# Kernel optimization log

Measured on AMD Instinct MI355X. Metric: run time of the kernel, lower is better.

Reference implementation:

```python
import jax, jax.numpy as jnp
import numpy as np
from jax import lax

DIM = 256
HEADS = 8


def dwconv3x3(x, w, b):
    # x: [B,C,H,W], w: [C,1,3,3] depthwise (groups=C), b: [C]
    y = lax.conv_general_dilated(
        x, w, window_strides=(1, 1), padding='SAME',
        dimension_numbers=('NCHW', 'OIHW', 'NCHW'),
        feature_group_count=x.shape[1])
    return y + b[None, :, None, None]


def conv1x1(x, w, b):
    # x: [B,Cin,H,W], w: [Cout,Cin], b: [Cout]
    return jnp.einsum('oc,bchw->bohw', w, x) + b[None, :, None, None]


def setup_inputs() -> dict:
    key = jax.random.key(0)
    ks = jax.random.split(key, 12)
    s = 0.05
    inp = {
        'x': jax.random.normal(ks[0], (4, DIM, 128, 128), dtype=jnp.float32),
        'q_w': jax.random.normal(ks[1], (DIM, 1, 3, 3), dtype=jnp.float32) * s,
        'q_b': jax.random.normal(ks[2], (DIM,), dtype=jnp.float32) * s,
        'k_w': jax.random.normal(ks[3], (DIM, 1, 3, 3), dtype=jnp.float32) * s,
        'k_b': jax.random.normal(ks[4], (DIM,), dtype=jnp.float32) * s,
        'v_w': jax.random.normal(ks[5], (DIM, 1, 3, 3), dtype=jnp.float32) * s,
        'v_b': jax.random.normal(ks[6], (DIM,), dtype=jnp.float32) * s,
        'out_w': jax.random.normal(ks[7], (DIM, DIM), dtype=jnp.float32) * s,
        'out_b': jax.random.normal(ks[8], (DIM,), dtype=jnp.float32) * s,
        'fusion_w': jax.random.normal(ks[9], (DIM, 2 * DIM), dtype=jnp.float32) * s,
        'fusion_b': jax.random.normal(ks[10], (DIM,), dtype=jnp.float32) * s,
        'temperature': jnp.ones((HEADS, 1, 1), dtype=jnp.float32),
        'gamma': jax.random.normal(ks[11], (1,), dtype=jnp.float32) * 0.1,
    }
    return inp


def reference(x, q_w, q_b, k_w, k_b, v_w, v_b, out_w, out_b,
              fusion_w, fusion_b, temperature, gamma):
    b, c, h, w = x.shape
    ch = c // HEADS  # channels per head (32)
    q = dwconv3x3(x, q_w, q_b).reshape(b, HEADS, ch, h * w)
    k = dwconv3x3(x, k_w, k_b).reshape(b, HEADS, ch, h * w)
    v = dwconv3x3(x, v_w, v_b).reshape(b, HEADS, ch, h * w)
    # channel-wise attention: [b, head, c, c]
    attn = jnp.einsum('bhcn,bhdn->bhcd', q, k) * temperature[None]
    attn = jax.nn.softmax(attn, axis=-1)
    out = jnp.einsum('bhcd,bhdn->bhcn', attn, v).reshape(b, c, h, w)
    out = conv1x1(out, out_w, out_b)
    fused = jnp.concatenate([out * gamma[0], x], axis=1)  # [b, 2c, h, w]
    return conv1x1(fused, fusion_w, fusion_b)
```

## Files before the change

### kernel.cpp

```cpp
#include <hip/hip_runtime.h>

typedef __attribute__((ext_vector_type(8))) short bf16x8;
typedef __attribute__((ext_vector_type(4))) float f32x4;

static __device__ __forceinline__ unsigned short f2bf(float f) {
  unsigned u = __builtin_bit_cast(unsigned, f);
  unsigned r = u + 0x7fffu + ((u >> 16) & 1u);
  return (unsigned short)(r >> 16);
}
static __device__ __forceinline__ unsigned pkbf(float a, float b) {
  return (unsigned)f2bf(a) | ((unsigned)f2bf(b) << 16);
}

__global__ __launch_bounds__(256) void kprep(
    const float* __restrict__ out_w, const float* __restrict__ out_b,
    const float* __restrict__ fusion_w, const float* __restrict__ fusion_b,
    const float* __restrict__ gamma,
    float* __restrict__ W1g, float* __restrict__ bias_tot,
    unsigned short* __restrict__ Wcat) {
  const int o = blockIdx.x;
  const int c = threadIdx.x;
  const float g = gamma[0];
  float acc = 0.f, bacc = 0.f;
  for (int t = 0; t < 256; ++t) {
    float fw = fusion_w[o*512 + t];
    acc  += fw * out_w[t*256 + c];
    bacc += fw * out_b[t];
  }
  W1g[o*256 + c] = g * acc;
  if (c == 0) bias_tot[o] = g * bacc + fusion_b[o];
  unsigned short w2b = f2bf(fusion_w[o*512 + 256 + c]);
  const int col = ((c >> 5) << 6) + 32 + (c & 31);
  for (int b = 0; b < 4; ++b)
    Wcat[((size_t)(b*256 + o))*512 + col] = w2b;
}

struct SmA { float xs[5184]; unsigned short qk[2][32][256]; };
union SmU { SmA a; unsigned short vx[256][72]; };

__global__ __launch_bounds__(256, 3) void k_qkv(
    const float* __restrict__ x,
    const float* __restrict__ q_w, const float* __restrict__ q_b,
    const float* __restrict__ k_w, const float* __restrict__ k_b,
    const float* __restrict__ v_w, const float* __restrict__ v_b,
    unsigned short* __restrict__ bx,
    float* __restrict__ gp)
{
  __shared__ SmU sm;
  const int t = blockIdx.x, h = blockIdx.y, b = blockIdx.z;
  const int tid = threadIdx.x;
  __builtin_assume(tid < 256);
  const int wv = tid >> 6, lane = tid & 63;
  const int w4 = __builtin_amdgcn_readfirstlane(wv);
  const int ty = t >> 3, tx = t & 7;
  const int y0 = ty * 16, x0 = tx * 16;
  const int py = lane >> 2, px0 = (lane & 3) * 4;

  float ra[21], rb[21];
  #pragma unroll
  for (int it = 0; it < 21; ++it) {
    int i = tid + it * 256;
    ra[it] = 0.f; rb[it] = 0.f;
    if (i < 5184) {
      int c = i / 324, r = i - c * 324;
      int yy = r / 18, xx = r - yy * 18;
      int gy = y0 + yy - 1, gx = x0 + xx - 1;
      if ((unsigned)gy < 128u && (unsigned)gx < 128u) {
        const float* p = x + (((size_t)(b * 256 + h * 32 + c)) * 128 + gy) * 128 + gx;
        ra[it] = p[0];
        rb[it] = p[16 * 16384];
      }
    }
  }

  uint2 vpack[2][4], xpack[2][4];
  #pragma unroll
  for (int pass = 0; pass < 2; ++pass) {
    #pragma unroll
    for (int it = 0; it < 21; ++it) {
      int i = tid + it * 256;
      if (i < 5184) sm.a.xs[i] = pass ? rb[it] : ra[it];
    }
    __syncthreads();

    const int cbase = h * 32 + pass * 16;
    float vvf[4][4], xxf[4][4];
    #pragma unroll
    for (int j = 0; j < 4; ++j) {
      const int cl = w4 * 4 + j;
      const int ch = cbase + cl;
      float wq[9], wk[9], wvv[9];
      #pragma unroll
      for (int i2 = 0; i2 < 9; ++i2) {
        wq[i2]  = q_w[ch * 9 + i2];
        wk[i2]  = k_w[ch * 9 + i2];
        wvv[i2] = v_w[ch * 9 + i2];
      }
      const float bq = q_b[ch], bk = k_b[ch], bv = v_b[ch];
      float win[3][6];
      #pragma unroll
      for (int r = 0; r < 3; ++r) {
        const float* xrow = &sm.a.xs[cl * 324 + (py + r) * 18 + px0];
        float2 a01 = *(const float2*)&xrow[0];
        float2 a23 = *(const float2*)&xrow[2];
        float2 a45 = *(const float2*)&xrow[4];
        win[r][0] = a01.x; win[r][1] = a01.y;
        win[r][2] = a23.x; win[r][3] = a23.y;
        win[r][4] = a45.x; win[r][5] = a45.y;
      }
      const int ah = pass * 16 + cl;
      float q4[4], k4[4];
      #pragma unroll
      for (int px = 0; px < 4; ++px) {
        float aq = bq, ak = bk, av = bv;
        #pragma unroll
        for (int r = 0; r < 3; ++r)
          #pragma unroll
          for (int cx = 0; cx < 3; ++cx) {
            float xv = win[r][px + cx];
            aq += wq[r * 3 + cx] * xv;
            ak += wk[r * 3 + cx] * xv;
            av += wvv[r * 3 + cx] * xv;
          }
        q4[px] = aq; k4[px] = ak;
        vvf[j][px] = av;
        xxf[j][px] = win[1][px + 1];
      }
      const int sw = (((lane >> 1) ^ (ah & 7)) << 3) + ((lane & 1) << 2);
      *(uint2*)&sm.a.qk[0][ah][sw] = make_uint2(pkbf(q4[0], q4[1]), pkbf(q4[2], q4[3]));
      *(uint2*)&sm.a.qk[1][ah][sw] = make_uint2(pkbf(k4[0], k4[1]), pkbf(k4[2], k4[3]));
    }
    #pragma unroll
    for (int px = 0; px < 4; ++px) {
      vpack[pass][px] = make_uint2(pkbf(vvf[0][px], vvf[1][px]), pkbf(vvf[2][px], vvf[3][px]));
      xpack[pass][px] = make_uint2(pkbf(xxf[0][px], xxf[1][px]), pkbf(xxf[2][px], xxf[3][px]));
    }
    __syncthreads();
  }

  const int qm = wv >> 1, qn = wv & 1;
  const int lrow = lane & 15, quad = lane >> 4;
  const int rowa = qm * 16 + lrow, rowb = qn * 16 + lrow;
  f32x4 acc = {0.f, 0.f, 0.f, 0.f};
  #pragma unroll
  for (int ks = 0; ks < 8; ++ks) {
    bf16x8 a  = *(const bf16x8*)&sm.a.qk[0][rowa][(((ks * 4 + quad) ^ (rowa & 7)) << 3)];
    bf16x8 bb = *(const bf16x8*)&sm.a.qk[1][rowb][(((ks * 4 + quad) ^ (rowb & 7)) << 3)];
    acc = __builtin_amdgcn_mfma_f32_16x16x32_bf16(a, bb, acc, 0, 0, 0);
  }
  float* gpb = gp + ((size_t)((b * 8 + h) * 64 + t)) * 1024;
  #pragma unroll
  for (int r = 0; r < 4; ++r)
    gpb[(qm * 16 + quad * 4 + r) * 32 + qn * 16 + lrow] = acc[r];

  __syncthreads();

  const int chi = wv >> 1, half = wv & 1;
  #pragma unroll
  for (int pass = 0; pass < 2; ++pass)
    #pragma unroll
    for (int px = 0; px < 4; ++px) {
      int n = py * 16 + px0 + px;
      int key = (n >> 3) & 7;
      int cv = pass * 2 + chi;
      int cx2 = 4 + pass * 2 + chi;
      *(uint2*)&sm.vx[n][((cv ^ key) << 3) + (half << 2)] = vpack[pass][px];
      *(uint2*)&sm.vx[n][((cx2 ^ key) << 3) + (half << 2)] = xpack[pass][px];
    }
  __syncthreads();

  #pragma unroll
  for (int it = 0; it < 8; ++it) {
    int n = it * 32 + (tid >> 3);
    int m = tid & 7;
    int key = (n >> 3) & 7;
    uint4 val = *(const uint4*)&sm.vx[n][((m ^ key) << 3)];
    int pyn = n >> 4, pxn = n & 15;
    int ng = (y0 + pyn) * 128 + x0 + pxn;
    *(uint4*)&bx[((size_t)b * 16384 + ng) * 512 + h * 64 + m * 8] = val;
  }
}

__global__ __launch_bounds__(1024) void k_red(
    const float* __restrict__ gp, float* __restrict__ gp2) {
  const int g = blockIdx.x, h = blockIdx.y, b = blockIdx.z;
  const int tid = threadIdx.x;
  const float* base = gp + ((size_t)((b * 8 + h) * 64 + g * 8)) * 1024;
  float s = 0.f;
  #pragma unroll
  for (int t = 0; t < 8; ++t) s += base[t * 1024 + tid];
  gp2[((size_t)((b * 8 + h) * 8 + g)) * 1024 + tid] = s;
}

__global__ __launch_bounds__(1024) void k_softmax(
    const float* __restrict__ gp2, const float* __restrict__ temp,
    float* __restrict__ attn) {
  const int h = blockIdx.x, b = blockIdx.y;
  const int tid = threadIdx.x;
  const int c = tid >> 5, d = tid & 31;
  const float* base = gp2 + ((size_t)((b*8 + h)*8))*1024;
  float s = 0.f;
  #pragma unroll
  for (int t = 0; t < 8; ++t) s += base[t*1024 + tid];
  s *= temp[h];
  __shared__ float ls[32][33];
  ls[c][d] = s;
  __syncthreads();
  float m = -1e30f;
  #pragma unroll
  for (int i = 0; i < 32; ++i) m = fmaxf(m, ls[c][i]);
  __syncthreads();
  float e = __expf(s - m);
  ls[c][d] = e;
  __syncthreads();
  float sum = 0.f;
  #pragma unroll
  for (int i = 0; i < 32; ++i) sum += ls[c][i];
  attn[((size_t)((b*8 + h)*32 + c))*32 + d] = e / sum;
}

__global__ __launch_bounds__(256) void k_compose(
    const float* __restrict__ W1g, const float* __restrict__ attn,
    unsigned short* __restrict__ Wcat) {
  const int o = blockIdx.x, b = blockIdx.y;
  const int e = threadIdx.x;
  const int h = e >> 5, d = e & 31;
  const float* ab = attn + ((size_t)((b*8 + h)*32))*32 + d;
  const float* wb = W1g + o*256 + h*32;
  float s = 0.f;
  #pragma unroll
  for (int c2 = 0; c2 < 32; ++c2) s += wb[c2] * ab[c2*32];
  Wcat[((size_t)(b*256 + o))*512 + ((e >> 5) << 6) + (e & 31)] = f2bf(s);
}

__global__ __launch_bounds__(256) void k_gemm(
    const unsigned short* __restrict__ Wcat,
    const unsigned short* __restrict__ bx,
    const float* __restrict__ bias_tot,
    float* __restrict__ out) {
  __shared__ unsigned short Al[256][40];
  __shared__ unsigned short Bl[64][40];
  const int nt = blockIdx.x, b = blockIdx.y;
  const int tid = threadIdx.x;
  const int wv = tid >> 6, lane = tid & 63;
  const int lrow = lane & 15, quad = lane >> 4;
  const int nbase = nt * 64;
  const unsigned short* Ab = Wcat + (size_t)b * 256 * 512;
  const unsigned short* Bb = bx + ((size_t)b * 16384 + nbase) * 512;
  f32x4 acc[4][4] = {};

  const int srow = tid >> 2;
  const int sq4 = tid & 3;
  for (int ks = 0; ks < 16; ++ks) {
    const int k0 = ks * 32;
    #pragma unroll
    for (int r = 0; r < 4; ++r) {
      int row = srow + r*64;
      uint4 v4 = *(const uint4*)(Ab + (size_t)row*512 + k0 + sq4*8);
      *(uint4*)&Al[row][sq4*8] = v4;
    }
    {
      uint4 v4 = *(const uint4*)(Bb + (size_t)srow*512 + k0 + sq4*8);
      *(uint4*)&Bl[srow][sq4*8] = v4;
    }
    __syncthreads();
    bf16x8 af[4], bfv[4];
    #pragma unroll
    for (int i = 0; i < 4; ++i)
      af[i] = *(const bf16x8*)&Al[wv*64 + i*16 + lrow][quad*8];
    #pragma unroll
    for (int j = 0; j < 4; ++j)
      bfv[j] = *(const bf16x8*)&Bl[j*16 + lrow][quad*8];
    #pragma unroll
    for (int i = 0; i < 4; ++i)
      #pragma unroll
      for (int j = 0; j < 4; ++j)
        acc[i][j] = __builtin_amdgcn_mfma_f32_16x16x32_bf16(af[i], bfv[j], acc[i][j], 0, 0, 0);
    __syncthreads();
  }
  #pragma unroll
  for (int i = 0; i < 4; ++i) {
    #pragma unroll
    for (int r = 0; r < 4; ++r) {
      const int o = wv*64 + i*16 + quad*4 + r;
      const float bias = bias_tot[o];
      #pragma unroll
      for (int j = 0; j < 4; ++j) {
        const int n = nbase + j*16 + lrow;
        out[((size_t)(b*256 + o))*16384 + n] = acc[i][j][r] + bias;
      }
    }
  }
}

extern "C" void kernel_launch(void* const* d_in, const int* in_sizes, int n_in,
                              void* d_out, int out_size, void* d_ws, size_t ws_size,
                              hipStream_t stream) {
  const float* x        = (const float*)d_in[0];
  const float* q_w      = (const float*)d_in[1];
  const float* q_b      = (const float*)d_in[2];
  const float* k_w      = (const float*)d_in[3];
  const float* k_b      = (const float*)d_in[4];
  const float* v_w      = (const float*)d_in[5];
  const float* v_b      = (const float*)d_in[6];
  const float* out_w    = (const float*)d_in[7];
  const float* out_b    = (const float*)d_in[8];
  const float* fusion_w = (const float*)d_in[9];
  const float* fusion_b = (const float*)d_in[10];
  const float* temp     = (const float*)d_in[11];
  const float* gamma    = (const float*)d_in[12];
  float* out = (float*)d_out;

  char* ws = (char*)d_ws;
  unsigned short* bx   = (unsigned short*)(ws);
  float* gp            = (float*)(ws + 67108864);
  float* attn          = (float*)(ws + 75497472);
  float* W1g           = (float*)(ws + 75628544);
  float* bias_tot      = (float*)(ws + 75890688);
  unsigned short* Wcat = (unsigned short*)(ws + 75891712);
  float* gp2           = (float*)(ws + 76940288);

  kprep<<<dim3(256), dim3(256), 0, stream>>>(out_w, out_b, fusion_w, fusion_b,
                                             gamma, W1g, bias_tot, Wcat);
  k_qkv<<<dim3(64, 8, 4), dim3(256), 0, stream>>>(x, q_w, q_b, k_w, k_b, v_w, v_b, bx, gp);
  k_red<<<dim3(8, 8, 4), dim3(1024), 0, stream>>>(gp, gp2);
  k_softmax<<<dim3(8, 4), dim3(1024), 0, stream>>>(gp2, temp, attn);
  k_compose<<<dim3(256, 4), dim3(256), 0, stream>>>(W1g, attn, Wcat);
  k_gemm<<<dim3(256, 4), dim3(256), 0, stream>>>(Wcat, bx, bias_tot, out);
}
```

Before: 228.5 us.

## Load conv windows directly from global memory and shrink LDS for higher occupancy

The depthwise QKV conv kernel no longer stages the haloed input tile in shared memory. Each thread reads its 3x6 window straight from global memory, with a templated interior/border split so interior tiles skip bounds checks. The V/X transpose buffer is halved and written out in two rounds, and launch bounds are raised to 4 blocks per CU. The intent is to cut LDS traffic, barriers and register pressure so more blocks fit per CU. In exchange it does redundant overlapping global loads that rely on the cache hierarchy, plus an extra pair of barriers in the store phase.

```diff
diff --git a/kernel.cpp b/kernel.cpp
--- a/kernel.cpp
+++ b/kernel.cpp
@@ -35,10 +35,100 @@
     Wcat[((size_t)(b*256 + o))*512 + col] = w2b;
 }
 
-struct SmA { float xs[5184]; unsigned short qk[2][32][256]; };
-union SmU { SmA a; unsigned short vx[256][72]; };
-
-__global__ __launch_bounds__(256, 3) void k_qkv(
+struct SmQK { unsigned short qk[2][32][256]; };
+union SmU { SmQK a; unsigned short vx[128][72]; };
+
+template<bool BORDER>
+static __device__ __forceinline__ void conv_passes(
+    const float* __restrict__ x,
+    const float* __restrict__ q_w, const float* __restrict__ q_b,
+    const float* __restrict__ k_w, const float* __restrict__ k_b,
+    const float* __restrict__ v_w, const float* __restrict__ v_b,
+    SmU& sm, int b, int h, int w4, int lane,
+    int y0, int x0, int py, int px0,
+    uint2 vpack[2][4], uint2 xpack[2][4]) {
+  const int gy_base = y0 + py - 1;
+  const int gxc = x0 + px0;
+  const bool vr0 = !BORDER || ((unsigned)gy_base < 128u);
+  const bool vr2 = !BORDER || ((unsigned)(gy_base + 2) < 128u);
+  const bool gl  = !BORDER || (gxc > 0);
+  const bool gr  = !BORDER || (gxc + 4 < 128);
+
+  #pragma unroll
+  for (int pass = 0; pass < 2; ++pass) {
+    const int cbase = h * 32 + pass * 16;
+    #pragma unroll
+    for (int j = 0; j < 4; ++j) {
+      const int cl = w4 * 4 + j;
+      const int ch = cbase + cl;
+      float wq[9], wk[9], wvv[9];
+      #pragma unroll
+      for (int i2 = 0; i2 < 9; ++i2) {
+        wq[i2]  = q_w[ch * 9 + i2];
+        wk[i2]  = k_w[ch * 9 + i2];
+        wvv[i2] = v_w[ch * 9 + i2];
+      }
+      const float bq = q_b[ch], bk = k_b[ch], bv = v_b[ch];
+      const float* p = x + (((size_t)(b * 256 + ch)) * 128 + gy_base) * 128 + gxc;
+      float win[3][6];
+      #pragma unroll
+      for (int r = 0; r < 3; ++r) {
+        const float* pr = p + r * 128;
+        const bool vr = (r == 0) ? vr0 : (r == 2 ? vr2 : true);
+        if (!BORDER) {
+          float4 m4 = *(const float4*)pr;
+          win[r][0] = pr[-1];
+          win[r][1] = m4.x; win[r][2] = m4.y; win[r][3] = m4.z; win[r][4] = m4.w;
+          win[r][5] = pr[4];
+        } else {
+          float4 m4 = vr ? *(const float4*)pr : make_float4(0.f, 0.f, 0.f, 0.f);
+          win[r][0] = (vr && gl) ? pr[-1] : 0.f;
+          win[r][1] = m4.x; win[r][2] = m4.y; win[r][3] = m4.z; win[r][4] = m4.w;
+          win[r][5] = (vr && gr) ? pr[4] : 0.f;
+        }
+      }
+      const int ah = pass * 16 + cl;
+      float q4[4], k4[4], v4[4];
+      #pragma unroll
+      for (int px = 0; px < 4; ++px) {
+        float aq = bq, ak = bk, av = bv;
+        #pragma unroll
+        for (int r = 0; r < 3; ++r)
+          #pragma unroll
+          for (int cx = 0; cx < 3; ++cx) {
+            float xv = win[r][px + cx];
+            aq += wq[r * 3 + cx] * xv;
+            ak += wk[r * 3 + cx] * xv;
+            av += wvv[r * 3 + cx] * xv;
+          }
+        q4[px] = aq; k4[px] = ak; v4[px] = av;
+      }
+      const int sw = (((lane >> 1) ^ (ah & 7)) << 3) + ((lane & 1) << 2);
+      *(uint2*)&sm.a.qk[0][ah][sw] = make_uint2(pkbf(q4[0], q4[1]), pkbf(q4[2], q4[3]));
+      *(uint2*)&sm.a.qk[1][ah][sw] = make_uint2(pkbf(k4[0], k4[1]), pkbf(k4[2], k4[3]));
+      if (j == 0 || j == 2) {
+        #pragma unroll
+        for (int px = 0; px < 4; ++px) {
+          if (j == 0) { vpack[pass][px].x = pkbf(v4[px], 0.f); xpack[pass][px].x = pkbf(win[1][px + 1], 0.f); }
+          else        { vpack[pass][px].y = pkbf(v4[px], 0.f); xpack[pass][px].y = pkbf(win[1][px + 1], 0.f); }
+        }
+      } else {
+        #pragma unroll
+        for (int px = 0; px < 4; ++px) {
+          if (j == 1) {
+            vpack[pass][px].x |= (unsigned)f2bf(v4[px]) << 16;
+            xpack[pass][px].x |= (unsigned)f2bf(win[1][px + 1]) << 16;
+          } else {
+            vpack[pass][px].y |= (unsigned)f2bf(v4[px]) << 16;
+            xpack[pass][px].y |= (unsigned)f2bf(win[1][px + 1]) << 16;
+          }
+        }
+      }
+    }
+  }
+}
+
+__global__ __launch_bounds__(256, 4) void k_qkv(
     const float* __restrict__ x,
     const float* __restrict__ q_w, const float* __restrict__ q_b,
     const float* __restrict__ k_w, const float* __restrict__ k_b,
@@ -55,88 +145,15 @@
   const int ty = t >> 3, tx = t & 7;
   const int y0 = ty * 16, x0 = tx * 16;
   const int py = lane >> 2, px0 = (lane & 3) * 4;
-
-  float ra[21], rb[21];
-  #pragma unroll
-  for (int it = 0; it < 21; ++it) {
-    int i = tid + it * 256;
-    ra[it] = 0.f; rb[it] = 0.f;
-    if (i < 5184) {
-      int c = i / 324, r = i - c * 324;
-      int yy = r / 18, xx = r - yy * 18;
-      int gy = y0 + yy - 1, gx = x0 + xx - 1;
-      if ((unsigned)gy < 128u && (unsigned)gx < 128u) {
-        const float* p = x + (((size_t)(b * 256 + h * 32 + c)) * 128 + gy) * 128 + gx;
-        ra[it] = p[0];
-        rb[it] = p[16 * 16384];
-      }
-    }
-  }
+  const bool border = (ty == 0) || (ty == 7) || (tx == 0) || (tx == 7);
 
   uint2 vpack[2][4], xpack[2][4];
-  #pragma unroll
-  for (int pass = 0; pass < 2; ++pass) {
-    #pragma unroll
-    for (int it = 0; it < 21; ++it) {
-      int i = tid + it * 256;
-      if (i < 5184) sm.a.xs[i] = pass ? rb[it] : ra[it];
-    }
-    __syncthreads();
-
-    const int cbase = h * 32 + pass * 16;
-    float vvf[4][4], xxf[4][4];
-    #pragma unroll
-    for (int j = 0; j < 4; ++j) {
-      const int cl = w4 * 4 + j;
-      const int ch = cbase + cl;
-      float wq[9], wk[9], wvv[9];
-      #pragma unroll
-      for (int i2 = 0; i2 < 9; ++i2) {
-        wq[i2]  = q_w[ch * 9 + i2];
-        wk[i2]  = k_w[ch * 9 + i2];
-        wvv[i2] = v_w[ch * 9 + i2];
-      }
-      const float bq = q_b[ch], bk = k_b[ch], bv = v_b[ch];
-      float win[3][6];
-      #pragma unroll
-      for (int r = 0; r < 3; ++r) {
-        const float* xrow = &sm.a.xs[cl * 324 + (py + r) * 18 + px0];
-        float2 a01 = *(const float2*)&xrow[0];
-        float2 a23 = *(const float2*)&xrow[2];
-        float2 a45 = *(const float2*)&xrow[4];
-        win[r][0] = a01.x; win[r][1] = a01.y;
-        win[r][2] = a23.x; win[r][3] = a23.y;
-        win[r][4] = a45.x; win[r][5] = a45.y;
-      }
-      const int ah = pass * 16 + cl;
-      float q4[4], k4[4];
-      #pragma unroll
-      for (int px = 0; px < 4; ++px) {
-        float aq = bq, ak = bk, av = bv;
-        #pragma unroll
-        for (int r = 0; r < 3; ++r)
-          #pragma unroll
-          for (int cx = 0; cx < 3; ++cx) {
-            float xv = win[r][px + cx];
-            aq += wq[r * 3 + cx] * xv;
-            ak += wk[r * 3 + cx] * xv;
-            av += wvv[r * 3 + cx] * xv;
-          }
-        q4[px] = aq; k4[px] = ak;
-        vvf[j][px] = av;
-        xxf[j][px] = win[1][px + 1];
-      }
-      const int sw = (((lane >> 1) ^ (ah & 7)) << 3) + ((lane & 1) << 2);
-      *(uint2*)&sm.a.qk[0][ah][sw] = make_uint2(pkbf(q4[0], q4[1]), pkbf(q4[2], q4[3]));
-      *(uint2*)&sm.a.qk[1][ah][sw] = make_uint2(pkbf(k4[0], k4[1]), pkbf(k4[2], k4[3]));
-    }
-    #pragma unroll
-    for (int px = 0; px < 4; ++px) {
-      vpack[pass][px] = make_uint2(pkbf(vvf[0][px], vvf[1][px]), pkbf(vvf[2][px], vvf[3][px]));
-      xpack[pass][px] = make_uint2(pkbf(xxf[0][px], xxf[1][px]), pkbf(xxf[2][px], xxf[3][px]));
-    }
-    __syncthreads();
-  }
+  if (border)
+    conv_passes<true >(x, q_w, q_b, k_w, k_b, v_w, v_b, sm, b, h, w4, lane, y0, x0, py, px0, vpack, xpack);
+  else
+    conv_passes<false>(x, q_w, q_b, k_w, k_b, v_w, v_b, sm, b, h, w4, lane, y0, x0, py, px0, vpack, xpack);
+
+  __syncthreads();
 
   const int qm = wv >> 1, qn = wv & 1;
   const int lrow = lane & 15, quad = lane >> 4;
@@ -157,27 +174,33 @@
 
   const int chi = wv >> 1, half = wv & 1;
   #pragma unroll
-  for (int pass = 0; pass < 2; ++pass)
-    #pragma unroll
-    for (int px = 0; px < 4; ++px) {
-      int n = py * 16 + px0 + px;
-      int key = (n >> 3) & 7;
-      int cv = pass * 2 + chi;
-      int cx2 = 4 + pass * 2 + chi;
-      *(uint2*)&sm.vx[n][((cv ^ key) << 3) + (half << 2)] = vpack[pass][px];
-      *(uint2*)&sm.vx[n][((cx2 ^ key) << 3) + (half << 2)] = xpack[pass][px];
-    }
-  __syncthreads();
-
-  #pragma unroll
-  for (int it = 0; it < 8; ++it) {
-    int n = it * 32 + (tid >> 3);
-    int m = tid & 7;
-    int key = (n >> 3) & 7;
-    uint4 val = *(const uint4*)&sm.vx[n][((m ^ key) << 3)];
-    int pyn = n >> 4, pxn = n & 15;
-    int ng = (y0 + pyn) * 128 + x0 + pxn;
-    *(uint4*)&bx[((size_t)b * 16384 + ng) * 512 + h * 64 + m * 8] = val;
+  for (int rr = 0; rr < 2; ++rr) {
+    if ((py >> 3) == rr) {
+      #pragma unroll
+      for (int pass = 0; pass < 2; ++pass)
+        #pragma unroll
+        for (int px = 0; px < 4; ++px) {
+          int nloc = (py & 7) * 16 + px0 + px;
+          int key = (nloc >> 3) & 7;
+          int cv = pass * 2 + chi;
+          int cx2 = 4 + pass * 2 + chi;
+          *(uint2*)&sm.vx[nloc][((cv ^ key) << 3) + (half << 2)] = vpack[pass][px];
+          *(uint2*)&sm.vx[nloc][((cx2 ^ key) << 3) + (half << 2)] = xpack[pass][px];
+        }
+    }
+    __syncthreads();
+    #pragma unroll
+    for (int it = 0; it < 4; ++it) {
+      int nloc = it * 32 + (tid >> 3);
+      int m = tid & 7;
+      int key = (nloc >> 3) & 7;
+      uint4 val = *(const uint4*)&sm.vx[nloc][((m ^ key) << 3)];
+      int n = rr * 128 + nloc;
+      int pyn = n >> 4, pxn = n & 15;
+      int ng = (y0 + pyn) * 128 + x0 + pxn;
+      *(uint4*)&bx[((size_t)b * 16384 + ng) * 512 + h * 64 + m * 8] = val;
+    }
+    __syncthreads();
   }
 }
 
```

Result: slower. 330.7 us (+44.7%).

## Read qkv conv windows straight from global memory and write V/X directly

Applied to the files above, without the earlier changes.

The LDS staging of the 18x18 halo tile is removed. Each thread now loads its own 3x6 window per channel directly from global memory with float4 loads plus edge scalars, relying on cache for halo reuse. The V and X bf16 values are written straight to global as 8-byte stores, replacing the LDS transpose and 16-byte coalesced store pass, which removes two barriers and shrinks shared memory to the qk buffer only. The tile index mapping is swapped so neighbouring blocks share columns, and the min-blocks launch bound is dropped. The cost is redundant global/L2 reads of halo rows and narrower, more scattered output stores.

```diff
diff --git a/kernel.cpp b/kernel.cpp
--- a/kernel.cpp
+++ b/kernel.cpp
@@ -35,10 +35,7 @@
     Wcat[((size_t)(b*256 + o))*512 + col] = w2b;
 }
 
-struct SmA { float xs[5184]; unsigned short qk[2][32][256]; };
-union SmU { SmA a; unsigned short vx[256][72]; };
-
-__global__ __launch_bounds__(256, 3) void k_qkv(
+__global__ __launch_bounds__(256) void k_qkv(
     const float* __restrict__ x,
     const float* __restrict__ q_w, const float* __restrict__ q_b,
     const float* __restrict__ k_w, const float* __restrict__ k_b,
@@ -46,49 +43,30 @@
     unsigned short* __restrict__ bx,
     float* __restrict__ gp)
 {
-  __shared__ SmU sm;
+  __shared__ __align__(16) unsigned short qk[2][32][256];
   const int t = blockIdx.x, h = blockIdx.y, b = blockIdx.z;
   const int tid = threadIdx.x;
   __builtin_assume(tid < 256);
   const int wv = tid >> 6, lane = tid & 63;
   const int w4 = __builtin_amdgcn_readfirstlane(wv);
-  const int ty = t >> 3, tx = t & 7;
+  const int ty = t & 7, tx = t >> 3;
   const int y0 = ty * 16, x0 = tx * 16;
   const int py = lane >> 2, px0 = (lane & 3) * 4;
 
-  float ra[21], rb[21];
-  #pragma unroll
-  for (int it = 0; it < 21; ++it) {
-    int i = tid + it * 256;
-    ra[it] = 0.f; rb[it] = 0.f;
-    if (i < 5184) {
-      int c = i / 324, r = i - c * 324;
-      int yy = r / 18, xx = r - yy * 18;
-      int gy = y0 + yy - 1, gx = x0 + xx - 1;
-      if ((unsigned)gy < 128u && (unsigned)gx < 128u) {
-        const float* p = x + (((size_t)(b * 256 + h * 32 + c)) * 128 + gy) * 128 + gx;
-        ra[it] = p[0];
-        rb[it] = p[16 * 16384];
-      }
-    }
-  }
-
-  uint2 vpack[2][4], xpack[2][4];
+  const int gy_base = y0 + py - 1;
+  const int gxc = x0 + px0;
+  const bool vr0 = (unsigned)gy_base < 128u;
+  const bool vr2 = (unsigned)(gy_base + 2) < 128u;
+  const bool gl  = gxc > 0;
+  const bool gr  = gxc + 4 < 128;
+
   #pragma unroll
   for (int pass = 0; pass < 2; ++pass) {
-    #pragma unroll
-    for (int it = 0; it < 21; ++it) {
-      int i = tid + it * 256;
-      if (i < 5184) sm.a.xs[i] = pass ? rb[it] : ra[it];
-    }
-    __syncthreads();
-
-    const int cbase = h * 32 + pass * 16;
-    float vvf[4][4], xxf[4][4];
+    uint2 vp[4], xp[4];
     #pragma unroll
     for (int j = 0; j < 4; ++j) {
-      const int cl = w4 * 4 + j;
-      const int ch = cbase + cl;
+      const int ah = pass * 16 + w4 * 4 + j;
+      const int ch = h * 32 + ah;
       float wq[9], wk[9], wvv[9];
       #pragma unroll
       for (int i2 = 0; i2 < 9; ++i2) {
@@ -97,18 +75,17 @@
         wvv[i2] = v_w[ch * 9 + i2];
       }
       const float bq = q_b[ch], bk = k_b[ch], bv = v_b[ch];
+      const float* p = x + (((size_t)(b * 256 + ch)) * 128 + gy_base) * 128 + gxc;
       float win[3][6];
       #pragma unroll
       for (int r = 0; r < 3; ++r) {
-        const float* xrow = &sm.a.xs[cl * 324 + (py + r) * 18 + px0];
-        float2 a01 = *(const float2*)&xrow[0];
-        float2 a23 = *(const float2*)&xrow[2];
-        float2 a45 = *(const float2*)&xrow[4];
-        win[r][0] = a01.x; win[r][1] = a01.y;
-        win[r][2] = a23.x; win[r][3] = a23.y;
-        win[r][4] = a45.x; win[r][5] = a45.y;
-      }
-      const int ah = pass * 16 + cl;
+        const float* pr = p + r * 128;
+        const bool vr = (r == 0) ? vr0 : (r == 2 ? vr2 : true);
+        float4 m4 = vr ? *(const float4*)pr : make_float4(0.f, 0.f, 0.f, 0.f);
+        win[r][0] = (vr && gl) ? pr[-1] : 0.f;
+        win[r][1] = m4.x; win[r][2] = m4.y; win[r][3] = m4.z; win[r][4] = m4.w;
+        win[r][5] = (vr && gr) ? pr[4] : 0.f;
+      }
       float q4[4], k4[4];
       #pragma unroll
       for (int px = 0; px < 4; ++px) {
@@ -123,20 +100,25 @@
             av += wvv[r * 3 + cx] * xv;
           }
         q4[px] = aq; k4[px] = ak;
-        vvf[j][px] = av;
-        xxf[j][px] = win[1][px + 1];
+        unsigned short vb = f2bf(av), xb = f2bf(win[1][px + 1]);
+        if (j == 0)      { vp[px].x = vb;                    xp[px].x = xb; }
+        else if (j == 1) { vp[px].x |= (unsigned)vb << 16;   xp[px].x |= (unsigned)xb << 16; }
+        else if (j == 2) { vp[px].y = vb;                    xp[px].y = xb; }
+        else             { vp[px].y |= (unsigned)vb << 16;   xp[px].y |= (unsigned)xb << 16; }
       }
       const int sw = (((lane >> 1) ^ (ah & 7)) << 3) + ((lane & 1) << 2);
-      *(uint2*)&sm.a.qk[0][ah][sw] = make_uint2(pkbf(q4[0], q4[1]), pkbf(q4[2], q4[3]));
-      *(uint2*)&sm.a.qk[1][ah][sw] = make_uint2(pkbf(k4[0], k4[1]), pkbf(k4[2], k4[3]));
-    }
+      *(uint2*)&qk[0][ah][sw] = make_uint2(pkbf(q4[0], q4[1]), pkbf(q4[2], q4[3]));
+      *(uint2*)&qk[1][ah][sw] = make_uint2(pkbf(k4[0], k4[1]), pkbf(k4[2], k4[3]));
+    }
+    size_t rowbase = ((size_t)b * 16384 + (size_t)(y0 + py) * 128 + x0 + px0) * 512
+                   + h * 64 + pass * 16 + w4 * 4;
     #pragma unroll
     for (int px = 0; px < 4; ++px) {
-      vpack[pass][px] = make_uint2(pkbf(vvf[0][px], vvf[1][px]), pkbf(vvf[2][px], vvf[3][px]));
-      xpack[pass][px] = make_uint2(pkbf(xxf[0][px], xxf[1][px]), pkbf(xxf[2][px], xxf[3][px]));
-    }
-    __syncthreads();
-  }
+      *(uint2*)&bx[rowbase + (size_t)px * 512]      = vp[px];
+      *(uint2*)&bx[rowbase + (size_t)px * 512 + 32] = xp[px];
+    }
+  }
+  __syncthreads();
 
   const int qm = wv >> 1, qn = wv & 1;
   const int lrow = lane & 15, quad = lane >> 4;
@@ -144,41 +126,14 @@
   f32x4 acc = {0.f, 0.f, 0.f, 0.f};
   #pragma unroll
   for (int ks = 0; ks < 8; ++ks) {
-    bf16x8 a  = *(const bf16x8*)&sm.a.qk[0][rowa][(((ks * 4 + quad) ^ (rowa & 7)) << 3)];
-    bf16x8 bb = *(const bf16x8*)&sm.a.qk[1][rowb][(((ks * 4 + quad) ^ (rowb & 7)) << 3)];
+    bf16x8 a  = *(const bf16x8*)&qk[0][rowa][(((ks * 4 + quad) ^ (rowa & 7)) << 3)];
+    bf16x8 bb = *(const bf16x8*)&qk[1][rowb][(((ks * 4 + quad) ^ (rowb & 7)) << 3)];
     acc = __builtin_amdgcn_mfma_f32_16x16x32_bf16(a, bb, acc, 0, 0, 0);
   }
   float* gpb = gp + ((size_t)((b * 8 + h) * 64 + t)) * 1024;
   #pragma unroll
   for (int r = 0; r < 4; ++r)
     gpb[(qm * 16 + quad * 4 + r) * 32 + qn * 16 + lrow] = acc[r];
-
-  __syncthreads();
-
-  const int chi = wv >> 1, half = wv & 1;
-  #pragma unroll
-  for (int pass = 0; pass < 2; ++pass)
-    #pragma unroll
-    for (int px = 0; px < 4; ++px) {
-      int n = py * 16 + px0 + px;
-      int key = (n >> 3) & 7;
-      int cv = pass * 2 + chi;
-      int cx2 = 4 + pass * 2 + chi;
-      *(uint2*)&sm.vx[n][((cv ^ key) << 3) + (half << 2)] = vpack[pass][px];
-      *(uint2*)&sm.vx[n][((cx2 ^ key) << 3) + (half << 2)] = xpack[pass][px];
-    }
-  __syncthreads();
-
-  #pragma unroll
-  for (int it = 0; it < 8; ++it) {
-    int n = it * 32 + (tid >> 3);
-    int m = tid & 7;
-    int key = (n >> 3) & 7;
-    uint4 val = *(const uint4*)&sm.vx[n][((m ^ key) << 3)];
-    int pyn = n >> 4, pxn = n & 15;
-    int ng = (y0 + pyn) * 128 + x0 + pxn;
-    *(uint4*)&bx[((size_t)b * 16384 + ng) * 512 + h * 64 + m * 8] = val;
-  }
 }
 
 __global__ __launch_bounds__(1024) void k_red(
```

After: 287.4 us. 1.26x slower.
